# Optimization experiments

Measured on AMD Instinct MI355X. Metric: run time of the kernel, lower is better.

Reference implementation:

```python
import jax, jax.numpy as jnp
import numpy as np

N_NODES = 100000
N_EDGES = 3200000
D_IN = 256
D_HID = 256
D_OUT = 64


def setup_inputs() -> dict:
    key = jax.random.key(0)
    k1, k2, k3, k4 = jax.random.split(key, 4)
    x = jax.random.normal(k1, (N_NODES, D_IN), dtype=jnp.float32)
    edge_index = jax.random.randint(k2, (2, N_EDGES), 0, N_NODES, dtype=jnp.int32)
    W1 = jax.random.normal(k3, (D_IN, D_HID), dtype=jnp.float32) / np.sqrt(D_IN)
    b1 = jnp.zeros((D_HID,), dtype=jnp.float32)
    W2 = jax.random.normal(k4, (D_HID, D_OUT), dtype=jnp.float32) / np.sqrt(D_HID)
    b2 = jnp.zeros((D_OUT,), dtype=jnp.float32)
    return {"x": x, "edge_index": edge_index, "W1": W1, "b1": b1, "W2": W2, "b2": b2}


def _gcn_conv(x, src, dst, norm, W, b, n_nodes):
    # dense linear transform, then normalized scatter-add aggregation
    h = x @ W  # [N, out]
    msg = norm[:, None] * h[src]  # gather + scale, [E+N, out]
    out = jax.ops.segment_sum(msg, dst, num_segments=n_nodes)
    return out + b


def reference(x, edge_index, W1, b1, W2, b2):
    n = x.shape[0]
    # add self-loops (PyG GCNConv default)
    loops = jnp.arange(n, dtype=edge_index.dtype)
    src = jnp.concatenate([edge_index[0], loops])
    dst = jnp.concatenate([edge_index[1], loops])
    # symmetric normalization deg^{-1/2}[src] * deg^{-1/2}[dst]
    deg = jax.ops.segment_sum(jnp.ones_like(src, dtype=x.dtype), dst, num_segments=n)
    dinv = jnp.where(deg > 0, jax.lax.rsqrt(jnp.maximum(deg, 1.0)), 0.0)
    norm = dinv[src] * dinv[dst]

    h = _gcn_conv(x, src, dst, norm, W1, b1, n)
    h = jax.nn.relu(h)
    # dropout is identity at inference
    h = _gcn_conv(h, src, dst, norm, W2, b2, n)
    return jax.nn.log_softmax(h, axis=1)
```

## Files before the change

kernel.cpp:

```cpp
#include <hip/hip_runtime.h>
#include <hip/hip_bf16.h>


typedef __bf16 bf16;
typedef bf16 bf16x4 __attribute__((ext_vector_type(4)));
typedef bf16 bf16x8 __attribute__((ext_vector_type(8)));
typedef float f32x4 __attribute__((ext_vector_type(4)));
typedef signed char s8;
typedef s8 s8x8 __attribute__((ext_vector_type(8)));

#define NBLK 256

__global__ __launch_bounds__(256) void k_b1(const int* __restrict__ edge, int E, int chunk,
                                            int NB, int* __restrict__ gcnt) {
    __shared__ int cnt[512];
    int tid = threadIdx.x;
    for (int i = tid; i < NB; i += 256) cnt[i] = 0;
    __syncthreads();
    int s = blockIdx.x * chunk, e = min(s + chunk, E);
    for (int i = s + tid; i < e; i += 256) atomicAdd(&cnt[edge[E + i] >> 9], 1);
    __syncthreads();
    for (int i = tid; i < NB; i += 256) gcnt[blockIdx.x * NB + i] = cnt[i];
}

__global__ void k_b2(const int* __restrict__ gcnt, int NB, int E, int* __restrict__ bstart) {
    __shared__ int col[256];
    int k = threadIdx.x;
    int sum = 0;
    if (k < NB)
        for (int b = 0; b < NBLK; ++b) sum += gcnt[b * NB + k];
    col[k] = sum;
    __syncthreads();
    for (int o = 1; o < 256; o <<= 1) {
        int v = (k >= o) ? col[k - o] : 0;
        __syncthreads();
        col[k] += v;
        __syncthreads();
    }
    if (k < NB) bstart[k] = col[k] - sum;
    if (k == 0) bstart[NB] = E;
}

__global__ void k_b2b(int* __restrict__ gcnt, int NB, const int* __restrict__ bstart) {
    __shared__ int col[256];
    int b = threadIdx.x;
    int k = blockIdx.x;
    int v = gcnt[b * NB + k];
    col[b] = v;
    __syncthreads();
    for (int o = 1; o < 256; o <<= 1) {
        int t = (b >= o) ? col[b - o] : 0;
        __syncthreads();
        col[b] += t;
        __syncthreads();
    }
    gcnt[b * NB + k] = bstart[k] + col[b] - v;
}

__global__ __launch_bounds__(256) void k_b3(const int* __restrict__ edge, int E, int chunk,
                                            int NB, const int* __restrict__ base,
                                            int* __restrict__ ebuf) {
    __shared__ int cnt[512];
    __shared__ int bs[512];
    int tid = threadIdx.x;
    for (int i = tid; i < NB; i += 256) {
        cnt[i] = 0;
        bs[i] = base[blockIdx.x * NB + i];
    }
    __syncthreads();
    int s = blockIdx.x * chunk, e = min(s + chunk, E);
    for (int i = s + tid; i < e; i += 256) {
        int sv = edge[i], dv = edge[E + i];
        int k = dv >> 9;
        int r = atomicAdd(&cnt[k], 1);
        ebuf[bs[k] + r] = sv | ((dv & 511) << 17);
    }
}

__global__ __launch_bounds__(256) void k_b45(const int* __restrict__ ebuf,
                                             const int* __restrict__ bstart, int n, int E,
                                             int NB, int* __restrict__ off,
                                             float* __restrict__ dinv) {
    __shared__ int cnt[512];
    __shared__ int red[256];
    int tid = threadIdx.x;
    int k = blockIdx.x;
    cnt[tid] = 0;
    cnt[tid + 256] = 0;
    __syncthreads();
    int s = bstart[k], e = bstart[k + 1];
    for (int i = s + tid; i < e; i += 256) atomicAdd(&cnt[(ebuf[i] >> 17) & 511], 1);
    __syncthreads();
    int c0 = cnt[tid * 2], c1 = cnt[tid * 2 + 1];
    int sum = c0 + c1;
    red[tid] = sum;
    __syncthreads();
    for (int o = 1; o < 256; o <<= 1) {
        int v = (tid >= o) ? red[tid - o] : 0;
        __syncthreads();
        red[tid] += v;
        __syncthreads();
    }
    int ex = red[tid] - sum;
    int base = k << 9;
    int g0 = base + tid * 2, g1 = g0 + 1;
    int o0 = s + ex, o1 = s + ex + c0;
    if (g0 < n) { off[g0] = o0; dinv[g0] = rsqrtf((float)(c0 + 1)); }
    else if (g0 == n) off[g0] = o0;
    if (g1 < n) { off[g1] = o1; dinv[g1] = rsqrtf((float)(c1 + 1)); }
    else if (g1 == n) off[g1] = o1;
    if (k == NB - 1 && tid == 0) off[n] = E;
}

__global__ __launch_bounds__(256) void k_b6(const int* __restrict__ ebuf,
                                            const int* __restrict__ bstart,
                                            const int* __restrict__ off,
                                            const float* __restrict__ dinv,
                                            const float* __restrict__ scale, int n,
                                            int2* __restrict__ pair) {
    __shared__ int cnt[512];
    __shared__ int offl[512];
    int tid = threadIdx.x;
    int k = blockIdx.x;
    int base = k << 9;
    cnt[tid] = 0;
    cnt[tid + 256] = 0;
    offl[tid] = (base + tid < n) ? off[base + tid] : 0;
    offl[tid + 256] = (base + 256 + tid < n) ? off[base + 256 + tid] : 0;
    __syncthreads();
    int s = bstart[k], e = bstart[k + 1];
    for (int i = s + tid; i < e; i += 256) {
        int pk = ebuf[i];
        int sv = pk & 0x1ffff;
        int node = (pk >> 17) & 511;
        int r = atomicAdd(&cnt[node], 1);
        float w = dinv[sv] * scale[sv];
        pair[offl[node] + r] = make_int2(sv, __float_as_int(w));
    }
}

__global__ __launch_bounds__(256) void k_quant(const float* __restrict__ x,
                                               unsigned char* __restrict__ xq,
                                               float* __restrict__ scale, int n) {
    int row = blockIdx.x * 4 + (threadIdx.x >> 6);
    int lane = threadIdx.x & 63;
    if (row >= n) return;
    f32x4 v = ((const f32x4*)x)[(size_t)row * 64 + lane];
    float m = fmaxf(fmaxf(fabsf(v[0]), fabsf(v[1])), fmaxf(fabsf(v[2]), fabsf(v[3])));
    for (int o = 32; o > 0; o >>= 1) m = fmaxf(m, __shfl_xor(m, o));
    m = fmaxf(m, 1e-20f);
    float inv = 127.0f / m;
    int b0 = (__float2int_rn(v[0] * inv) + 128) & 255;
    int b1 = (__float2int_rn(v[1] * inv) + 128) & 255;
    int b2 = (__float2int_rn(v[2] * inv) + 128) & 255;
    int b3 = (__float2int_rn(v[3] * inv) + 128) & 255;
    ((int*)xq)[(size_t)row * 64 + lane] = b0 | (b1 << 8) | (b2 << 16) | (b3 << 24);
    if (lane == 0) scale[row] = m / 127.0f;
}

__global__ __launch_bounds__(256) void k_quant2(const bf16* __restrict__ tb,
                                                const float* __restrict__ scale,
                                                s8* __restrict__ tq,
                                                float* __restrict__ tscale,
                                                float* __restrict__ r2, int n) {
    int t = blockIdx.x * 256 + threadIdx.x;
    int row = t >> 3;
    int l8 = t & 7;
    if (row >= n) return;
    bf16x8 v = ((const bf16x8*)tb)[(size_t)row * 8 + l8];
    float f[8], m = 0.0f;
#pragma unroll
    for (int j = 0; j < 8; ++j) { f[j] = (float)v[j]; m = fmaxf(m, fabsf(f[j])); }
    for (int o = 4; o > 0; o >>= 1) m = fmaxf(m, __shfl_xor(m, o));
    m = fmaxf(m, 1e-20f);
    float inv = 127.0f / m;
    int lo = 0, hi = 0;
#pragma unroll
    for (int j = 0; j < 4; ++j) lo |= (__float2int_rn(f[j] * inv) & 255) << (8 * j);
#pragma unroll
    for (int j = 0; j < 4; ++j) hi |= (__float2int_rn(f[4 + j] * inv) & 255) << (8 * j);
    ((int2*)tq)[(size_t)row * 8 + l8] = make_int2(lo, hi);
    if (l8 == 0) {
        float s = m / 127.0f;
        tscale[row] = s;
        r2[row] = s / scale[row];
    }
}

__global__ void k_wt(const float* __restrict__ W, bf16* __restrict__ Wt, int NC) {
    int nc = blockIdx.x;
    int k = threadIdx.x;
    Wt[nc * 256 + k] = (bf16)W[k * NC + nc];
}

__device__ __forceinline__ void acc16(float a[16], uint4 t, float w, float& wsum) {
    wsum += w;
    unsigned u0 = t.x, u1 = t.y, u2 = t.z, u3 = t.w;
    a[0]  += w * (float)(u0 & 255u);
    a[1]  += w * (float)((u0 >> 8) & 255u);
    a[2]  += w * (float)((u0 >> 16) & 255u);
    a[3]  += w * (float)(u0 >> 24);
    a[4]  += w * (float)(u1 & 255u);
    a[5]  += w * (float)((u1 >> 8) & 255u);
    a[6]  += w * (float)((u1 >> 16) & 255u);
    a[7]  += w * (float)(u1 >> 24);
    a[8]  += w * (float)(u2 & 255u);
    a[9]  += w * (float)((u2 >> 8) & 255u);
    a[10] += w * (float)((u2 >> 16) & 255u);
    a[11] += w * (float)(u2 >> 24);
    a[12] += w * (float)(u3 & 255u);
    a[13] += w * (float)((u3 >> 8) & 255u);
    a[14] += w * (float)((u3 >> 16) & 255u);
    a[15] += w * (float)(u3 >> 24);
}

__global__ __launch_bounds__(256) void k_agg1(const unsigned char* __restrict__ xq,
                                              const float* __restrict__ scale,
                                              const int* __restrict__ off,
                                              const int2* __restrict__ pair,
                                              const float* __restrict__ dinv,
                                              bf16* __restrict__ ax, int n) {
    int wv = blockIdx.x * 4 + (threadIdx.x >> 6);
    int lane = threadIdx.x & 63;
    int node = wv * 4 + (lane >> 4);
    int l16 = lane & 15;
    if (node >= n) return;
    int s0 = off[node], s1 = off[node + 1];
    float dv = dinv[node];
    float a[16] = {};
    float wsum = 0.0f;
    uint4 xs = *(const uint4*)(xq + (size_t)node * 256 + l16 * 16);
    acc16(a, xs, dv * scale[node], wsum);
    int e = s0;
    for (; e + 4 <= s1; e += 4) {
        int2 p[4];
#pragma unroll
        for (int q = 0; q < 4; ++q) p[q] = pair[e + q];
        uint4 t[4];
#pragma unroll
        for (int q = 0; q < 4; ++q)
            t[q] = *(const uint4*)(xq + (size_t)p[q].x * 256 + l16 * 16);
#pragma unroll
        for (int q = 0; q < 4; ++q) acc16(a, t[q], __int_as_float(p[q].y), wsum);
    }
    for (; e < s1; ++e) {
        int2 p = pair[e];
        uint4 t = *(const uint4*)(xq + (size_t)p.x * 256 + l16 * 16);
        acc16(a, t, __int_as_float(p.y), wsum);
    }
    float c = 128.0f * wsum;
    bf16x8 o0, o1;
#pragma unroll
    for (int j = 0; j < 8; ++j) o0[j] = (bf16)((a[j] - c) * dv);
#pragma unroll
    for (int j = 0; j < 8; ++j) o1[j] = (bf16)((a[8 + j] - c) * dv);
    ((bf16x8*)ax)[(size_t)node * 32 + l16 * 2] = o0;
    ((bf16x8*)ax)[(size_t)node * 32 + l16 * 2 + 1] = o1;
}

__global__ __launch_bounds__(256) void k_gemmp(const bf16* __restrict__ A,
                                               const bf16* __restrict__ Bt,
                                               const float* __restrict__ bias,
                                               bf16* __restrict__ C, int n) {
    __shared__ __align__(16) bf16 As[4 * 64 * 8];
    __shared__ __align__(16) bf16 Bs[16 * 64 * 8];
    int tid = threadIdx.x;
    int bm = blockIdx.x * 64;
    int w = tid >> 6, lane = tid & 63;

    int r = tid >> 2;
    int cq = tid & 3;
    int a_idx = (((r >> 4) * 64) + cq * 16 + (r & 15)) * 8;
    int arow = bm + r; if (arow > n - 1) arow = n - 1;

    f32x4 acc[16] = {};

    for (int k0 = 0; k0 < 256; k0 += 32) {
        __syncthreads();
        uint4 av = *(const uint4*)(A + (size_t)arow * 256 + k0 + cq * 8);
        *(uint4*)(As + a_idx) = av;
#pragma unroll
        for (int rep = 0; rep < 4; ++rep) {
            int r2 = rep * 64 + r;
            uint4 bv = *(const uint4*)(Bt + (size_t)r2 * 256 + k0 + cq * 8);
            *(uint4*)(Bs + (((r2 >> 4) * 64) + cq * 16 + (r2 & 15)) * 8) = bv;
        }
        __syncthreads();
        bf16x8 af = *(const bf16x8*)(As + (w * 64 + lane) * 8);
#pragma unroll
        for (int ct = 0; ct < 16; ++ct) {
            bf16x8 bfr = *(const bf16x8*)(Bs + (ct * 64 + lane) * 8);
            acc[ct] = __builtin_amdgcn_mfma_f32_16x16x32_bf16(af, bfr, acc[ct], 0, 0, 0);
        }
    }

    int colb = lane & 15, rowq = lane >> 4;
#pragma unroll
    for (int ct = 0; ct < 16; ++ct) {
        int col = ct * 16 + colb;
        float bv = bias[col];
#pragma unroll
        for (int rr = 0; rr < 4; ++rr) {
            int row = bm + w * 16 + rowq * 4 + rr;
            if (row < n) {
                float v = acc[ct][rr] + bv;
                C[(size_t)row * 256 + col] = (bf16)(v > 0.0f ? v : 0.0f);
            }
        }
    }
}

__global__ __launch_bounds__(256) void k_gemm2(const bf16* __restrict__ A,
                                               const bf16* __restrict__ Bt,
                                               bf16* __restrict__ C, int n) {
    __shared__ __align__(16) bf16 As[4 * 64 * 8];
    __shared__ __align__(16) bf16 Bs[4 * 64 * 8];
    int tid = threadIdx.x;
    int bm = blockIdx.x * 64;
    int w = tid >> 6, lane = tid & 63;
    int wm = w >> 1, wn = w & 1;

    int r = tid >> 2;
    int cq = tid & 3;
    int lds_idx = (((r >> 4) * 64) + cq * 16 + (r & 15)) * 8;
    int arow = bm + r; if (arow > n - 1) arow = n - 1;

    f32x4 acc[2][2] = {};

    for (int k0 = 0; k0 < 256; k0 += 32) {
        __syncthreads();
        uint4 av = *(const uint4*)(A + (size_t)arow * 256 + k0 + cq * 8);
        uint4 bv = *(const uint4*)(Bt + (size_t)r * 256 + k0 + cq * 8);
        *(uint4*)(As + lds_idx) = av;
        *(uint4*)(Bs + lds_idx) = bv;
        __syncthreads();
#pragma unroll
        for (int i = 0; i < 2; ++i) {
            bf16x8 af = *(const bf16x8*)(As + ((wm * 2 + i) * 64 + lane) * 8);
#pragma unroll
            for (int j = 0; j < 2; ++j) {
                bf16x8 bfr = *(const bf16x8*)(Bs + ((wn * 2 + j) * 64 + lane) * 8);
                acc[i][j] = __builtin_amdgcn_mfma_f32_16x16x32_bf16(af, bfr, acc[i][j], 0, 0, 0);
            }
        }
    }

    int colb = lane & 15, rowq = lane >> 4;
#pragma unroll
    for (int i = 0; i < 2; ++i) {
#pragma unroll
        for (int j = 0; j < 2; ++j) {
            int col = wn * 32 + j * 16 + colb;
#pragma unroll
            for (int rr = 0; rr < 4; ++rr) {
                int row = bm + wm * 32 + i * 16 + rowq * 4 + rr;
                if (row < n) C[(size_t)row * 64 + col] = (bf16)acc[i][j][rr];
            }
        }
    }
}

__global__ __launch_bounds__(256) void k_agg2(const s8* __restrict__ tq,
                                              const float* __restrict__ tscale,
                                              const float* __restrict__ r2,
                                              const int* __restrict__ off,
                                              const int2* __restrict__ pair,
                                              const float* __restrict__ dinv,
                                              const float* __restrict__ b2,
                                              float* __restrict__ out, int n) {
    int wv = blockIdx.x * 4 + (threadIdx.x >> 6);
    int lane = threadIdx.x & 63;
    int node = wv * 8 + (lane >> 3);
    int l8 = lane & 7;
    if (node >= n) return;
    int s0 = off[node], s1 = off[node + 1];
    float dv = dinv[node];
    const s8x8* T = (const s8x8*)tq;
    s8x8 ts = T[(size_t)node * 8 + l8];
    float ws = dv * tscale[node];
    float a[8];
#pragma unroll
    for (int j = 0; j < 8; ++j) a[j] = ws * (float)ts[j];
    int e = s0;
    for (; e + 4 <= s1; e += 4) {
        int2 p[4];
#pragma unroll
        for (int q = 0; q < 4; ++q) p[q] = pair[e + q];
        float sc[4];
#pragma unroll
        for (int q = 0; q < 4; ++q) sc[q] = r2[p[q].x];
        s8x8 tv[4];
#pragma unroll
        for (int q = 0; q < 4; ++q) tv[q] = T[(size_t)p[q].x * 8 + l8];
#pragma unroll
        for (int q = 0; q < 4; ++q) {
            float w = __int_as_float(p[q].y) * sc[q];
#pragma unroll
            for (int j = 0; j < 8; ++j) a[j] += w * (float)tv[q][j];
        }
    }
    for (; e < s1; ++e) {
        int2 p = pair[e];
        float w = __int_as_float(p.y) * r2[p.x];
        s8x8 tv = T[(size_t)p.x * 8 + l8];
#pragma unroll
        for (int j = 0; j < 8; ++j) a[j] += w * (float)tv[j];
    }
    const float4* B2 = (const float4*)b2;
    float4 bv0 = B2[l8 * 2], bv1 = B2[l8 * 2 + 1];
    a[0] = a[0] * dv + bv0.x; a[1] = a[1] * dv + bv0.y;
    a[2] = a[2] * dv + bv0.z; a[3] = a[3] * dv + bv0.w;
    a[4] = a[4] * dv + bv1.x; a[5] = a[5] * dv + bv1.y;
    a[6] = a[6] * dv + bv1.z; a[7] = a[7] * dv + bv1.w;
    float m = a[0];
#pragma unroll
    for (int j = 1; j < 8; ++j) m = fmaxf(m, a[j]);
    for (int o = 4; o > 0; o >>= 1) m = fmaxf(m, __shfl_xor(m, o));
    float s = 0.0f;
#pragma unroll
    for (int j = 0; j < 8; ++j) s += __expf(a[j] - m);
    for (int o = 4; o > 0; o >>= 1) s += __shfl_xor(s, o);
    float ls = m + __logf(s);
    f32x4 o0, o1;
    o0[0] = a[0] - ls; o0[1] = a[1] - ls; o0[2] = a[2] - ls; o0[3] = a[3] - ls;
    o1[0] = a[4] - ls; o1[1] = a[5] - ls; o1[2] = a[6] - ls; o1[3] = a[7] - ls;
    f32x4* O = (f32x4*)out;
    O[(size_t)node * 16 + l8 * 2] = o0;
    O[(size_t)node * 16 + l8 * 2 + 1] = o1;
}

extern "C" void kernel_launch(void* const* d_in, const int* in_sizes, int n_in,
                              void* d_out, int out_size, void* d_ws, size_t ws_size,
                              hipStream_t stream) {
    const float* x   = (const float*)d_in[0];
    const int*  edge = (const int*)d_in[1];
    const float* W1  = (const float*)d_in[2];
    const float* b1  = (const float*)d_in[3];
    const float* W2  = (const float*)d_in[4];
    const float* b2  = (const float*)d_in[5];
    float* out = (float*)d_out;

    int n = in_sizes[0] / 256;
    int E = in_sizes[1] / 2;
    int NB = (n + 511) >> 9;
    int chunk = (E + NBLK - 1) / NBLK;

    char* ws = (char*)d_ws;
    auto alloc = [&](size_t bytes) -> char* {
        char* p = ws;
        ws += (bytes + 255) & ~(size_t)255;
        return p;
    };
    int*   gcnt   = (int*)alloc((size_t)NBLK * NB * 4);
    int*   bstart = (int*)alloc((size_t)(NB + 1) * 4);
    int*   ebuf   = (int*)alloc((size_t)E * 4);
    float* dinv   = (float*)alloc((size_t)n * 4);
    int*   off    = (int*)alloc((size_t)(n + 1) * 4);
    int2*  pair   = (int2*)alloc((size_t)E * 8);
    unsigned char* xq = (unsigned char*)alloc((size_t)n * 256);
    float* scale  = (float*)alloc((size_t)n * 4);
    bf16*  ax     = (bf16*)alloc((size_t)n * 256 * 2);
    bf16*  h1     = (bf16*)alloc((size_t)n * 256 * 2);
    bf16*  tb     = (bf16*)alloc((size_t)n * 64 * 2);
    s8*    tq     = (s8*)alloc((size_t)n * 64);
    float* tscale = (float*)alloc((size_t)n * 4);
    float* r2     = (float*)alloc((size_t)n * 4);
    bf16*  W1t    = (bf16*)alloc(256 * 256 * 2);
    bf16*  W2t    = (bf16*)alloc(64 * 256 * 2);

    k_quant<<<(n + 3) / 4, 256, 0, stream>>>(x, xq, scale, n);

    k_b1<<<NBLK, 256, 0, stream>>>(edge, E, chunk, NB, gcnt);
    k_b2<<<1, 256, 0, stream>>>(gcnt, NB, E, bstart);
    k_b2b<<<NB, 256, 0, stream>>>(gcnt, NB, bstart);
    k_b3<<<NBLK, 256, 0, stream>>>(edge, E, chunk, NB, gcnt, ebuf);
    k_b45<<<NB, 256, 0, stream>>>(ebuf, bstart, n, E, NB, off, dinv);
    k_b6<<<NB, 256, 0, stream>>>(ebuf, bstart, off, dinv, scale, n, pair);

    k_wt<<<256, 256, 0, stream>>>(W1, W1t, 256);
    k_wt<<<64, 256, 0, stream>>>(W2, W2t, 64);

    k_agg1<<<(n + 15) / 16, 256, 0, stream>>>(xq, scale, off, pair, dinv, ax, n);
    k_gemmp<<<(n + 63) / 64, 256, 0, stream>>>(ax, W1t, b1, h1, n);

    k_gemm2<<<(n + 63) / 64, 256, 0, stream>>>(h1, W2t, tb, n);
    k_quant2<<<(n * 8 + 255) / 256, 256, 0, stream>>>(tb, scale, tq, tscale, r2, n);
    k_agg2<<<(n + 31) / 32, 256, 0, stream>>>(tq, tscale, r2, off, pair, dinv, b2, out, n);
}
```

Before: 562.5 us.

## Assign one wavefront per node in both aggregations, splitting edges across lane groups

Both gather-aggregation kernels now map a whole 64-lane wavefront to one destination node instead of packing several nodes per wave. The edges of that node are split across lane groups, four groups in agg1 and eight in agg2, and the partial sums are combined with cross-lane shuffles. Only one lane group writes the result. The second-layer int8 values become unsigned with a +128 offset, corrected through the weight sum, so agg2 can reuse the same unpack-and-accumulate path as agg1. The aim is more memory-level parallelism per node and less load imbalance from uneven degrees. In exchange, the kernels do extra shuffle reductions, tail iterations leave some lanes idle, and four times more blocks are launched.

```diff
diff --git a/kernel.cpp b/kernel.cpp
--- a/kernel.cpp
+++ b/kernel.cpp
@@ -7,7 +7,6 @@
 typedef bf16 bf16x8 __attribute__((ext_vector_type(8)));
 typedef float f32x4 __attribute__((ext_vector_type(4)));
 typedef signed char s8;
-typedef s8 s8x8 __attribute__((ext_vector_type(8)));
 
 #define NBLK 256
 
@@ -160,7 +159,7 @@
 
 __global__ __launch_bounds__(256) void k_quant2(const bf16* __restrict__ tb,
                                                 const float* __restrict__ scale,
-                                                s8* __restrict__ tq,
+                                                unsigned char* __restrict__ tq,
                                                 float* __restrict__ tscale,
                                                 float* __restrict__ r2, int n) {
     int t = blockIdx.x * 256 + threadIdx.x;
@@ -176,9 +175,9 @@
     float inv = 127.0f / m;
     int lo = 0, hi = 0;
 #pragma unroll
-    for (int j = 0; j < 4; ++j) lo |= (__float2int_rn(f[j] * inv) & 255) << (8 * j);
-#pragma unroll
-    for (int j = 0; j < 4; ++j) hi |= (__float2int_rn(f[4 + j] * inv) & 255) << (8 * j);
+    for (int j = 0; j < 4; ++j) lo |= ((__float2int_rn(f[j] * inv) + 128) & 255) << (8 * j);
+#pragma unroll
+    for (int j = 0; j < 4; ++j) hi |= ((__float2int_rn(f[4 + j] * inv) + 128) & 255) << (8 * j);
     ((int2*)tq)[(size_t)row * 8 + l8] = make_int2(lo, hi);
     if (l8 == 0) {
         float s = m / 127.0f;
@@ -214,15 +213,28 @@
     a[15] += w * (float)(u3 >> 24);
 }
 
+__device__ __forceinline__ void acc8(float a[8], int2 t, float w, float& wsum) {
+    wsum += w;
+    unsigned u0 = (unsigned)t.x, u1 = (unsigned)t.y;
+    a[0] += w * (float)(u0 & 255u);
+    a[1] += w * (float)((u0 >> 8) & 255u);
+    a[2] += w * (float)((u0 >> 16) & 255u);
+    a[3] += w * (float)(u0 >> 24);
+    a[4] += w * (float)(u1 & 255u);
+    a[5] += w * (float)((u1 >> 8) & 255u);
+    a[6] += w * (float)((u1 >> 16) & 255u);
+    a[7] += w * (float)(u1 >> 24);
+}
+
 __global__ __launch_bounds__(256) void k_agg1(const unsigned char* __restrict__ xq,
                                               const float* __restrict__ scale,
                                               const int* __restrict__ off,
                                               const int2* __restrict__ pair,
                                               const float* __restrict__ dinv,
                                               bf16* __restrict__ ax, int n) {
-    int wv = blockIdx.x * 4 + (threadIdx.x >> 6);
+    int node = blockIdx.x * 4 + (threadIdx.x >> 6);
     int lane = threadIdx.x & 63;
-    int node = wv * 4 + (lane >> 4);
+    int qt = lane >> 4;
     int l16 = lane & 15;
     if (node >= n) return;
     int s0 = off[node], s1 = off[node + 1];
@@ -230,32 +242,43 @@
     float a[16] = {};
     float wsum = 0.0f;
     uint4 xs = *(const uint4*)(xq + (size_t)node * 256 + l16 * 16);
-    acc16(a, xs, dv * scale[node], wsum);
+    acc16(a, xs, (qt == 0) ? dv * scale[node] : 0.0f, wsum);
     int e = s0;
-    for (; e + 4 <= s1; e += 4) {
+    for (; e + 16 <= s1; e += 16) {
         int2 p[4];
 #pragma unroll
-        for (int q = 0; q < 4; ++q) p[q] = pair[e + q];
+        for (int i = 0; i < 4; ++i) p[i] = pair[e + 4 * i + qt];
         uint4 t[4];
 #pragma unroll
-        for (int q = 0; q < 4; ++q)
-            t[q] = *(const uint4*)(xq + (size_t)p[q].x * 256 + l16 * 16);
-#pragma unroll
-        for (int q = 0; q < 4; ++q) acc16(a, t[q], __int_as_float(p[q].y), wsum);
-    }
-    for (; e < s1; ++e) {
-        int2 p = pair[e];
+        for (int i = 0; i < 4; ++i)
+            t[i] = *(const uint4*)(xq + (size_t)p[i].x * 256 + l16 * 16);
+#pragma unroll
+        for (int i = 0; i < 4; ++i) acc16(a, t[i], __int_as_float(p[i].y), wsum);
+    }
+    for (; e < s1; e += 4) {
+        int idx = e + qt;
+        bool on = idx < s1;
+        int2 p = pair[on ? idx : s0];
         uint4 t = *(const uint4*)(xq + (size_t)p.x * 256 + l16 * 16);
-        acc16(a, t, __int_as_float(p.y), wsum);
-    }
+        acc16(a, t, on ? __int_as_float(p.y) : 0.0f, wsum);
+    }
+#pragma unroll
+    for (int j = 0; j < 16; ++j) {
+        a[j] += __shfl_xor(a[j], 16);
+        a[j] += __shfl_xor(a[j], 32);
+    }
+    wsum += __shfl_xor(wsum, 16);
+    wsum += __shfl_xor(wsum, 32);
     float c = 128.0f * wsum;
-    bf16x8 o0, o1;
-#pragma unroll
-    for (int j = 0; j < 8; ++j) o0[j] = (bf16)((a[j] - c) * dv);
-#pragma unroll
-    for (int j = 0; j < 8; ++j) o1[j] = (bf16)((a[8 + j] - c) * dv);
-    ((bf16x8*)ax)[(size_t)node * 32 + l16 * 2] = o0;
-    ((bf16x8*)ax)[(size_t)node * 32 + l16 * 2 + 1] = o1;
+    if (qt == 0) {
+        bf16x8 o0, o1;
+#pragma unroll
+        for (int j = 0; j < 8; ++j) o0[j] = (bf16)((a[j] - c) * dv);
+#pragma unroll
+        for (int j = 0; j < 8; ++j) o1[j] = (bf16)((a[8 + j] - c) * dv);
+        ((bf16x8*)ax)[(size_t)node * 32 + l16 * 2] = o0;
+        ((bf16x8*)ax)[(size_t)node * 32 + l16 * 2 + 1] = o1;
+    }
 }
 
 __global__ __launch_bounds__(256) void k_gemmp(const bf16* __restrict__ A,
@@ -360,7 +383,7 @@
     }
 }
 
-__global__ __launch_bounds__(256) void k_agg2(const s8* __restrict__ tq,
+__global__ __launch_bounds__(256) void k_agg2(const unsigned char* __restrict__ tq,
                                               const float* __restrict__ tscale,
                                               const float* __restrict__ r2,
                                               const int* __restrict__ off,
@@ -368,50 +391,51 @@
                                               const float* __restrict__ dinv,
                                               const float* __restrict__ b2,
                                               float* __restrict__ out, int n) {
-    int wv = blockIdx.x * 4 + (threadIdx.x >> 6);
+    int node = blockIdx.x * 4 + (threadIdx.x >> 6);
     int lane = threadIdx.x & 63;
-    int node = wv * 8 + (lane >> 3);
+    int oct = lane >> 3;
     int l8 = lane & 7;
     if (node >= n) return;
     int s0 = off[node], s1 = off[node + 1];
     float dv = dinv[node];
-    const s8x8* T = (const s8x8*)tq;
-    s8x8 ts = T[(size_t)node * 8 + l8];
-    float ws = dv * tscale[node];
-    float a[8];
-#pragma unroll
-    for (int j = 0; j < 8; ++j) a[j] = ws * (float)ts[j];
+    const int2* T = (const int2*)tq;
+    float a[8] = {};
+    float wsum = 0.0f;
+    int2 ts = T[(size_t)node * 8 + l8];
+    acc8(a, ts, (oct == 0) ? dv * tscale[node] : 0.0f, wsum);
     int e = s0;
-    for (; e + 4 <= s1; e += 4) {
-        int2 p[4];
-#pragma unroll
-        for (int q = 0; q < 4; ++q) p[q] = pair[e + q];
-        float sc[4];
-#pragma unroll
-        for (int q = 0; q < 4; ++q) sc[q] = r2[p[q].x];
-        s8x8 tv[4];
-#pragma unroll
-        for (int q = 0; q < 4; ++q) tv[q] = T[(size_t)p[q].x * 8 + l8];
-#pragma unroll
-        for (int q = 0; q < 4; ++q) {
-            float w = __int_as_float(p[q].y) * sc[q];
-#pragma unroll
-            for (int j = 0; j < 8; ++j) a[j] += w * (float)tv[q][j];
-        }
-    }
-    for (; e < s1; ++e) {
-        int2 p = pair[e];
-        float w = __int_as_float(p.y) * r2[p.x];
-        s8x8 tv = T[(size_t)p.x * 8 + l8];
-#pragma unroll
-        for (int j = 0; j < 8; ++j) a[j] += w * (float)tv[j];
-    }
+    for (; e + 16 <= s1; e += 16) {
+        int2 p0 = pair[e + oct], p1 = pair[e + 8 + oct];
+        float sc0 = r2[p0.x], sc1 = r2[p1.x];
+        int2 t0 = T[(size_t)p0.x * 8 + l8];
+        int2 t1 = T[(size_t)p1.x * 8 + l8];
+        acc8(a, t0, __int_as_float(p0.y) * sc0, wsum);
+        acc8(a, t1, __int_as_float(p1.y) * sc1, wsum);
+    }
+    for (; e < s1; e += 8) {
+        int idx = e + oct;
+        bool on = idx < s1;
+        int2 p = pair[on ? idx : s0];
+        float w = on ? __int_as_float(p.y) * r2[p.x] : 0.0f;
+        int2 t = T[(size_t)p.x * 8 + l8];
+        acc8(a, t, w, wsum);
+    }
+#pragma unroll
+    for (int j = 0; j < 8; ++j) {
+        a[j] += __shfl_xor(a[j], 8);
+        a[j] += __shfl_xor(a[j], 16);
+        a[j] += __shfl_xor(a[j], 32);
+    }
+    wsum += __shfl_xor(wsum, 8);
+    wsum += __shfl_xor(wsum, 16);
+    wsum += __shfl_xor(wsum, 32);
+    float c = 128.0f * wsum;
     const float4* B2 = (const float4*)b2;
     float4 bv0 = B2[l8 * 2], bv1 = B2[l8 * 2 + 1];
-    a[0] = a[0] * dv + bv0.x; a[1] = a[1] * dv + bv0.y;
-    a[2] = a[2] * dv + bv0.z; a[3] = a[3] * dv + bv0.w;
-    a[4] = a[4] * dv + bv1.x; a[5] = a[5] * dv + bv1.y;
-    a[6] = a[6] * dv + bv1.z; a[7] = a[7] * dv + bv1.w;
+    a[0] = (a[0] - c) * dv + bv0.x; a[1] = (a[1] - c) * dv + bv0.y;
+    a[2] = (a[2] - c) * dv + bv0.z; a[3] = (a[3] - c) * dv + bv0.w;
+    a[4] = (a[4] - c) * dv + bv1.x; a[5] = (a[5] - c) * dv + bv1.y;
+    a[6] = (a[6] - c) * dv + bv1.z; a[7] = (a[7] - c) * dv + bv1.w;
     float m = a[0];
 #pragma unroll
     for (int j = 1; j < 8; ++j) m = fmaxf(m, a[j]);
@@ -421,12 +445,14 @@
     for (int j = 0; j < 8; ++j) s += __expf(a[j] - m);
     for (int o = 4; o > 0; o >>= 1) s += __shfl_xor(s, o);
     float ls = m + __logf(s);
-    f32x4 o0, o1;
-    o0[0] = a[0] - ls; o0[1] = a[1] - ls; o0[2] = a[2] - ls; o0[3] = a[3] - ls;
-    o1[0] = a[4] - ls; o1[1] = a[5] - ls; o1[2] = a[6] - ls; o1[3] = a[7] - ls;
-    f32x4* O = (f32x4*)out;
-    O[(size_t)node * 16 + l8 * 2] = o0;
-    O[(size_t)node * 16 + l8 * 2 + 1] = o1;
+    if (oct == 0) {
+        f32x4 o0, o1;
+        o0[0] = a[0] - ls; o0[1] = a[1] - ls; o0[2] = a[2] - ls; o0[3] = a[3] - ls;
+        o1[0] = a[4] - ls; o1[1] = a[5] - ls; o1[2] = a[6] - ls; o1[3] = a[7] - ls;
+        f32x4* O = (f32x4*)out;
+        O[(size_t)node * 16 + l8 * 2] = o0;
+        O[(size_t)node * 16 + l8 * 2 + 1] = o1;
+    }
 }
 
 extern "C" void kernel_launch(void* const* d_in, const int* in_sizes, int n_in,
@@ -462,7 +488,7 @@
     bf16*  ax     = (bf16*)alloc((size_t)n * 256 * 2);
     bf16*  h1     = (bf16*)alloc((size_t)n * 256 * 2);
     bf16*  tb     = (bf16*)alloc((size_t)n * 64 * 2);
-    s8*    tq     = (s8*)alloc((size_t)n * 64);
+    unsigned char* tq = (unsigned char*)alloc((size_t)n * 64);
     float* tscale = (float*)alloc((size_t)n * 4);
     float* r2     = (float*)alloc((size_t)n * 4);
     bf16*  W1t    = (bf16*)alloc(256 * 256 * 2);
@@ -480,10 +506,10 @@
     k_wt<<<256, 256, 0, stream>>>(W1, W1t, 256);
     k_wt<<<64, 256, 0, stream>>>(W2, W2t, 64);
 
-    k_agg1<<<(n + 15) / 16, 256, 0, stream>>>(xq, scale, off, pair, dinv, ax, n);
+    k_agg1<<<(n + 3) / 4, 256, 0, stream>>>(xq, scale, off, pair, dinv, ax, n);
     k_gemmp<<<(n + 63) / 64, 256, 0, stream>>>(ax, W1t, b1, h1, n);
 
     k_gemm2<<<(n + 63) / 64, 256, 0, stream>>>(h1, W2t, tb, n);
     k_quant2<<<(n * 8 + 255) / 256, 256, 0, stream>>>(tb, scale, tq, tscale, r2, n);
-    k_agg2<<<(n + 31) / 32, 256, 0, stream>>>(tq, tscale, r2, off, pair, dinv, b2, out, n);
-}
+    k_agg2<<<(n + 3) / 4, 256, 0, stream>>>(tq, tscale, r2, off, pair, dinv, b2, out, n);
+}
```

Result: slower. 590.4 us (+5.0%).
